# Optimization experiments

Hardware: AMD Instinct MI355X
Metric: run time of the kernel (lower is better)

Reference implementation:

```python
import jax, jax.numpy as jnp
import numpy as np

D_MODEL = 512
N_STATE = 64
EMB_DIM = 512
LN_EPS = 1e-5


def setup_inputs() -> dict:
    key = jax.random.key(0)
    ks = jax.random.split(key, 12)
    B, L, d, N, e = 8, 2048, D_MODEL, N_STATE, EMB_DIM
    x = jax.random.normal(ks[0], (B, L, d), dtype=jnp.float32)
    emb = jax.random.normal(ks[1], (B, e), dtype=jnp.float32)
    # S4D kernel params
    A_real = -0.5 * jnp.ones((d, N), dtype=jnp.float32)
    A_imag = jnp.pi * jnp.broadcast_to(jnp.arange(N, dtype=jnp.float32)[None, :], (d, N))
    C = jax.random.normal(ks[2], (d, N, 2), dtype=jnp.float32) * 0.5
    dt_min, dt_max = 0.001, 0.1
    log_dt = jax.random.uniform(ks[3], (d,), dtype=jnp.float32) * (np.log(dt_max) - np.log(dt_min)) + np.log(dt_min)
    B_ssm = jnp.ones((d, N), dtype=jnp.float32)  # buffer, treated as constant
    # block params
    D_skip = jax.random.normal(ks[4], (d,), dtype=jnp.float32) * 0.01
    ln_gamma = jnp.ones((d,), dtype=jnp.float32)
    ln_beta = jnp.zeros((d,), dtype=jnp.float32)
    lim_out = 1.0 / np.sqrt(d)
    W_out = jax.random.uniform(ks[5], (2 * d, d), dtype=jnp.float32, minval=-lim_out, maxval=lim_out)
    b_out = jax.random.uniform(ks[6], (2 * d,), dtype=jnp.float32, minval=-lim_out, maxval=lim_out)
    lim_f = 1.0 / np.sqrt(e)
    W_film = jax.random.uniform(ks[7], (2 * d, e), dtype=jnp.float32, minval=-lim_f, maxval=lim_f)
    b_film = jax.random.uniform(ks[8], (2 * d,), dtype=jnp.float32, minval=-lim_f, maxval=lim_f)
    return dict(x=x, emb=emb, A_real=A_real, A_imag=A_imag, C=C, log_dt=log_dt,
                B_ssm=B_ssm, D_skip=D_skip, ln_gamma=ln_gamma, ln_beta=ln_beta,
                W_out=W_out, b_out=b_out, W_film=W_film, b_film=b_film)


def reference(x, emb, A_real, A_imag, C, log_dt, B_ssm, D_skip, ln_gamma, ln_beta,
              W_out, b_out, W_film, b_film):
    Bsz, L, d = x.shape
    residual = x
    # LayerNorm
    mu = jnp.mean(x, axis=-1, keepdims=True)
    var = jnp.mean((x - mu) ** 2, axis=-1, keepdims=True)
    xn = (x - mu) * jax.lax.rsqrt(var + LN_EPS) * ln_gamma + ln_beta
    # S4D kernel: K[d,l] = Re( sum_n (C*B)[d,n] * exp(dt*A)[d,n]**l ) * dt[d]
    dt = jnp.exp(log_dt)                                 # (d,)
    A = A_real + 1j * A_imag                             # (d,N)
    dtA = A * dt[:, None]                                # (d,N)
    Cc = (C[..., 0] + 1j * C[..., 1]) * B_ssm            # (d,N) complex
    l = jnp.arange(L, dtype=jnp.float32)
    powers = jnp.exp(dtA[:, :, None] * l)                # (d,N,L) complex, A_bar**l
    K = jnp.einsum('dn,dnl->dl', Cc, powers).real * dt[:, None]  # (d,L)
    # FFT convolution (circular over 2L -> linear)
    x_t = jnp.transpose(xn, (0, 2, 1))                   # (B,d,L)
    K_f = jnp.fft.rfft(K, n=2 * L)                       # (d,L+1)
    x_f = jnp.fft.rfft(x_t, n=2 * L)                     # (B,d,L+1)
    y = jnp.fft.irfft(K_f[None] * x_f, n=2 * L)[..., :L] # (B,d,L)
    y = y + x_t * D_skip[None, :, None]
    y = jnp.transpose(y, (0, 2, 1))                      # (B,L,d)
    # FiLM conditioning
    film = jax.nn.silu(emb) @ W_film.T + b_film          # (B,2d)
    scale, shift = jnp.split(film, 2, axis=-1)
    y = y * (1.0 + scale[:, None, :]) + shift[:, None, :]
    # out_proj: Linear(d,2d) + GLU
    proj = y @ W_out.T + b_out                           # (B,L,2d)
    a, g = jnp.split(proj, 2, axis=-1)
    y = a * jax.nn.sigmoid(g)
    return residual + y
```

## Files before the change

kernel.cpp:

```cpp
#include <hip/hip_runtime.h>
#include <math.h>

typedef __attribute__((ext_vector_type(8))) short bf8v;
typedef __attribute__((ext_vector_type(4))) float f4v;

union BF8 { bf8v v; unsigned short e[8]; };

__device__ __forceinline__ float bf2f(unsigned short u) {
  union { unsigned int i; float f; } c; c.i = ((unsigned int)u) << 16; return c.f;
}
__device__ __forceinline__ unsigned short f2bf(float f) {
  union { float f; unsigned int i; } c; c.f = f;
  return (unsigned short)((c.i + 0x7fffu + ((c.i >> 16) & 1u)) >> 16);
}

__global__ __launch_bounds__(64) void ln_kernel(const float* __restrict__ x,
    const float* __restrict__ gamma, const float* __restrict__ beta,
    unsigned short* __restrict__ xn) {
  const int row = blockIdx.x;
  const int lane = threadIdx.x;
  const float4* xr = (const float4*)(x + (size_t)row * 512);
  const float4 v0 = xr[lane * 2], v1 = xr[lane * 2 + 1];
  float s  = v0.x + v0.y + v0.z + v0.w + v1.x + v1.y + v1.z + v1.w;
  float sq = v0.x*v0.x + v0.y*v0.y + v0.z*v0.z + v0.w*v0.w
           + v1.x*v1.x + v1.y*v1.y + v1.z*v1.z + v1.w*v1.w;
  #pragma unroll
  for (int off = 32; off >= 1; off >>= 1) {
    s  += __shfl_xor(s, off);
    sq += __shfl_xor(sq, off);
  }
  const float mu   = s * (1.f / 512.f);
  const float var  = sq * (1.f / 512.f) - mu * mu;
  const float rstd = rsqrtf(var + 1e-5f);
  const float4* gp = (const float4*)gamma + lane * 2;
  const float4* bp = (const float4*)beta  + lane * 2;
  const float4 g0 = gp[0], g1 = gp[1], bb0 = bp[0], bb1 = bp[1];
  const float o0 = (v0.x - mu) * rstd * g0.x + bb0.x;
  const float o1 = (v0.y - mu) * rstd * g0.y + bb0.y;
  const float o2 = (v0.z - mu) * rstd * g0.z + bb0.z;
  const float o3 = (v0.w - mu) * rstd * g0.w + bb0.w;
  const float o4 = (v1.x - mu) * rstd * g1.x + bb1.x;
  const float o5 = (v1.y - mu) * rstd * g1.y + bb1.y;
  const float o6 = (v1.z - mu) * rstd * g1.z + bb1.z;
  const float o7 = (v1.w - mu) * rstd * g1.w + bb1.w;
  uint4 pk;
  pk.x = (unsigned)f2bf(o0) | ((unsigned)f2bf(o1) << 16);
  pk.y = (unsigned)f2bf(o2) | ((unsigned)f2bf(o3) << 16);
  pk.z = (unsigned)f2bf(o4) | ((unsigned)f2bf(o5) << 16);
  pk.w = (unsigned)f2bf(o6) | ((unsigned)f2bf(o7) << 16);
  ((uint4*)(xn + (size_t)row * 512))[lane] = pk;
}

__global__ __launch_bounds__(256) void film_kernel(const float* __restrict__ emb,
    const float* __restrict__ Wf, const float* __restrict__ bfm,
    float* __restrict__ film) {
  const int gw = blockIdx.x * 4 + (threadIdx.x >> 6);
  const int lane = threadIdx.x & 63;
  const int b = gw >> 10, j = gw & 1023;
  const float4* ep = (const float4*)(emb + (size_t)b * 512) + lane * 2;
  const float4* wp = (const float4*)(Wf + (size_t)j * 512) + lane * 2;
  float acc = 0.f;
  #pragma unroll
  for (int i = 0; i < 2; i++) {
    const float4 e = ep[i], w = wp[i];
    acc += (e.x / (1.f + __expf(-e.x))) * w.x;
    acc += (e.y / (1.f + __expf(-e.y))) * w.y;
    acc += (e.z / (1.f + __expf(-e.z))) * w.z;
    acc += (e.w / (1.f + __expf(-e.w))) * w.w;
  }
  #pragma unroll
  for (int off = 32; off >= 1; off >>= 1) acc += __shfl_xor(acc, off);
  if (lane == 0) film[(size_t)b * 1024 + j] = acc + bfm[j];
}

__global__ __launch_bounds__(256) void wcvt_kernel(const float* __restrict__ W,
    unsigned short* __restrict__ Wb) {
  const int i = blockIdx.x * 256 + threadIdx.x;
  const float4 v = ((const float4*)W)[i];
  uint2 pk;
  pk.x = (unsigned)f2bf(v.x) | ((unsigned)f2bf(v.y) << 16);
  pk.y = (unsigned)f2bf(v.z) | ((unsigned)f2bf(v.w) << 16);
  ((uint2*)Wb)[i] = pk;
}

__global__ __launch_bounds__(256) void tr_kernel(const unsigned short* __restrict__ in,
    unsigned short* __restrict__ out, int R, int C) {
  __shared__ __align__(16) unsigned short t[64 * 72];
  const int c0 = blockIdx.x * 64, r0 = blockIdx.y * 64;
  const int tid = threadIdx.x;
  #pragma unroll
  for (int i = 0; i < 2; i++) {
    const int idx = tid + i * 256;
    const int r = idx >> 3, q = idx & 7;
    const uint4 v = *(const uint4*)(in + (size_t)(r0 + r) * C + c0 + q * 8);
    *(uint4*)&t[r * 72 + ((q ^ (r >> 3)) * 8)] = v;
  }
  __syncthreads();
  #pragma unroll
  for (int i = 0; i < 2; i++) {
    const int idx = tid + i * 256;
    const int c = idx >> 3, g = idx & 7;
    union { unsigned short s[8]; uint4 u; } pk;
    #pragma unroll
    for (int j = 0; j < 8; j++)
      pk.s[j] = t[(g * 8 + j) * 72 + (((c >> 3) ^ g) * 8) + (c & 7)];
    *(uint4*)(out + (size_t)(c0 + c) * R + r0 + g * 8) = pk.u;
  }
}

__global__ __launch_bounds__(256) void ktab_kernel(const float* __restrict__ A_real,
    const float* __restrict__ A_imag, const float* __restrict__ Cc,
    const float* __restrict__ log_dt, const float* __restrict__ B_ssm,
    const float* __restrict__ D_skip, float* __restrict__ Kt) {
  const int d = blockIdx.x * 4 + (threadIdx.x >> 6);
  const int n = threadIdx.x & 63;
  const int dn = d * 64 + n;
  const float dt = __expf(log_dt[d]);
  const float er = __expf(dt * A_real[dn]);
  float sw, cw; __sincosf(dt * A_imag[dn], &sw, &cw);
  const float wre = er * cw, wim = er * sw;
  const float bs = B_ssm[dn] * dt;
  float pre = Cc[dn * 2] * bs, pim = Cc[dn * 2 + 1] * bs;
  const float dsk = D_skip[d];
  for (int tau = 0; tau < 64; tau++) {
    float r = pre;
    #pragma unroll
    for (int off = 32; off >= 1; off >>= 1) r += __shfl_xor(r, off);
    if (n == 0) Kt[d * 64 + tau] = (tau == 0) ? (r + dsk) : r;
    const float nre = pre * wre - pim * wim;
    const float nim = pre * wim + pim * wre;
    pre = nre; pim = nim;
  }
}

__global__ __launch_bounds__(256, 1) void ssm_kernel(
    const unsigned short* __restrict__ xT,
    const float* __restrict__ A_real, const float* __restrict__ A_imag,
    const float* __restrict__ Cc, const float* __restrict__ log_dt,
    const float* __restrict__ B_ssm, const float* __restrict__ Kt,
    const float* __restrict__ film, unsigned short* __restrict__ y2) {
  extern __shared__ char smem[];
  unsigned int*   Eb  = (unsigned int*)smem;
  unsigned short* Ibr = (unsigned short*)(smem + 64 * 258 * 4);
  unsigned short* Ibi = Ibr + 256 * 72;

  const int d = blockIdx.x;
  const int tid = threadIdx.x;
  const int wv = tid >> 6, lane = tid & 63;
  const int n15 = lane & 15, quad = lane >> 4;
  const int j0 = wv * 64;
  const float dt = __expf(log_dt[d]);

  bf8v Xf[4][2];
  #pragma unroll
  for (int ct = 0; ct < 4; ct++)
    #pragma unroll
    for (int kq = 0; kq < 2; kq++) {
      const int j = j0 + ct * 16 + n15;
      Xf[ct][kq] = *(const bf8v*)(xT + (size_t)d * 16384 + j * 64 + kq * 32 + quad * 8);
    }

  {
    f4v Er[4][4], Ei[4][4];
    #pragma unroll
    for (int a = 0; a < 4; a++)
      #pragma unroll
      for (int b2 = 0; b2 < 4; b2++) { Er[a][b2] = (f4v){0,0,0,0}; Ei[a][b2] = (f4v){0,0,0,0}; }
    #pragma unroll
    for (int mt = 0; mt < 4; mt++) {
      const int n = mt * 16 + n15;
      const float ar = dt * A_real[d * 64 + n], ai = dt * A_imag[d * 64 + n];
      #pragma unroll
      for (int kq = 0; kq < 2; kq++) {
        BF8 pr, pi;
        #pragma unroll
        for (int j = 0; j < 8; j++) {
          const float k = (float)(63 - (kq * 32 + quad * 8 + j));
          const float ex = __expf(ar * k);
          float sn, cs; __sincosf(ai * k, &sn, &cs);
          pr.e[j] = f2bf(ex * cs);
          pi.e[j] = f2bf(ex * sn);
        }
        #pragma unroll
        for (int ct = 0; ct < 4; ct++) {
          Er[mt][ct] = __builtin_amdgcn_mfma_f32_16x16x32_bf16(pr.v, Xf[ct][kq], Er[mt][ct], 0, 0, 0);
          Ei[mt][ct] = __builtin_amdgcn_mfma_f32_16x16x32_bf16(pi.v, Xf[ct][kq], Ei[mt][ct], 0, 0, 0);
        }
      }
    }
    #pragma unroll
    for (int mt = 0; mt < 4; mt++)
      #pragma unroll
      for (int ct = 0; ct < 4; ct++)
        #pragma unroll
        for (int i = 0; i < 4; i++) {
          const int row = mt * 16 + quad * 4 + i;
          const int col = j0 + ct * 16 + n15;
          Eb[row * 258 + col] =
              (unsigned)f2bf(Er[mt][ct][i]) | ((unsigned)f2bf(Ei[mt][ct][i]) << 16);
        }
  }
  __syncthreads();

  {
    const int n = tid & 63, bp = tid >> 6;
    const int dn = d * 64 + n;
    const float ex = __expf(dt * A_real[dn] * 64.f);
    float sn, cs; __sincosf(dt * A_imag[dn] * 64.f, &sn, &cs);
    const float w64re = ex * cs, w64im = ex * sn;
    #pragma unroll
    for (int half = 0; half < 2; half++) {
      const int b = bp + half * 4;
      float str = 0.f, sti = 0.f;
      for (int c = 0; c < 32; c++) {
        const int j = b * 32 + c;
        Ibr[j * 72 + n] = f2bf(str);
        Ibi[j * 72 + n] = f2bf(sti);
        const unsigned e = Eb[n * 258 + j];
        const float er2 = bf2f((unsigned short)(e & 0xffffu));
        const float ei2 = bf2f((unsigned short)(e >> 16));
        const float nr = er2 + w64re * str - w64im * sti;
        const float ni = ei2 + w64re * sti + w64im * str;
        str = nr; sti = ni;
      }
    }
  }
  __syncthreads();

  f4v Y[4][4];
  #pragma unroll
  for (int a = 0; a < 4; a++)
    #pragma unroll
    for (int b2 = 0; b2 < 4; b2++) Y[a][b2] = (f4v){0,0,0,0};

  #pragma unroll
  for (int mt = 0; mt < 4; mt++) {
    const int t = mt * 16 + n15;
    #pragma unroll
    for (int kq = 0; kq < 2; kq++) {
      BF8 tf;
      #pragma unroll
      for (int j = 0; j < 8; j++) {
        const int s = kq * 32 + quad * 8 + j;
        tf.e[j] = (s <= t) ? f2bf(Kt[d * 64 + (t - s)]) : (unsigned short)0;
      }
      #pragma unroll
      for (int ct = 0; ct < 4; ct++)
        Y[mt][ct] = __builtin_amdgcn_mfma_f32_16x16x32_bf16(tf.v, Xf[ct][kq], Y[mt][ct], 0, 0, 0);
    }
  }

  #pragma unroll
  for (int kq = 0; kq < 2; kq++) {
    float arj[8], aij[8], c0j[8], c1j[8];
    #pragma unroll
    for (int j = 0; j < 8; j++) {
      const int dn = d * 64 + kq * 32 + quad * 8 + j;
      arj[j] = dt * A_real[dn];
      aij[j] = dt * A_imag[dn];
      const float bs = B_ssm[dn] * dt;
      c0j[j] = Cc[dn * 2] * bs;
      c1j[j] = Cc[dn * 2 + 1] * bs;
    }
    bf8v irf[4], iif[4];
    #pragma unroll
    for (int ct = 0; ct < 4; ct++) {
      const int j = j0 + ct * 16 + n15;
      irf[ct] = *(const bf8v*)&Ibr[j * 72 + kq * 32 + quad * 8];
      iif[ct] = *(const bf8v*)&Ibi[j * 72 + kq * 32 + quad * 8];
    }
    #pragma unroll
    for (int mt = 0; mt < 4; mt++) {
      const int t = mt * 16 + n15;
      BF8 mr, mi;
      #pragma unroll
      for (int j = 0; j < 8; j++) {
        const float k = (float)(t + 1);
        const float ex = __expf(arj[j] * k);
        float sn, cs; __sincosf(aij[j] * k, &sn, &cs);
        mr.e[j] = f2bf(ex * (c0j[j] * cs - c1j[j] * sn));
        mi.e[j] = f2bf(-ex * (c0j[j] * sn + c1j[j] * cs));
      }
      #pragma unroll
      for (int ct = 0; ct < 4; ct++) {
        Y[mt][ct] = __builtin_amdgcn_mfma_f32_16x16x32_bf16(mr.v, irf[ct], Y[mt][ct], 0, 0, 0);
        Y[mt][ct] = __builtin_amdgcn_mfma_f32_16x16x32_bf16(mi.v, iif[ct], Y[mt][ct], 0, 0, 0);
      }
    }
  }

  #pragma unroll
  for (int ct = 0; ct < 4; ct++) {
    const int j = j0 + ct * 16 + n15;
    const int b = j >> 5;
    const float scl = 1.f + film[b * 1024 + d];
    const float shf = film[b * 1024 + 512 + d];
    #pragma unroll
    for (int mt = 0; mt < 4; mt++) {
      union { unsigned short s[4]; uint2 u; } pk;
      #pragma unroll
      for (int i = 0; i < 4; i++)
        pk.s[i] = f2bf(fmaf(Y[mt][ct][i], scl, shf));
      *(uint2*)(y2 + (size_t)d * 16384 + j * 64 + mt * 16 + quad * 4) = pk.u;
    }
  }
}

__global__ __launch_bounds__(256) void gemm_kernel(
    const unsigned short* __restrict__ y2n, const unsigned short* __restrict__ Wb,
    const float* __restrict__ bo, const float* __restrict__ x,
    float* __restrict__ out) {
  __shared__ __align__(16) unsigned short Al[64 * 48];
  __shared__ __align__(16) unsigned short Bl[128 * 48];
  const int m0 = blockIdx.x * 64, ct = blockIdx.y;
  const int tid = threadIdx.x;
  const int wv = tid >> 6, lane = tid & 63;
  const int n15 = lane & 15, quad = lane >> 4;
  f4v acc[2][4];
  #pragma unroll
  for (int hh = 0; hh < 2; hh++)
    #pragma unroll
    for (int t4 = 0; t4 < 4; t4++) acc[hh][t4] = (f4v){0.f, 0.f, 0.f, 0.f};

  const int ar  = tid >> 2;
  const int ak  = (tid & 3) * 8;
  const int cc0 = tid >> 2;
  const int ks  = (tid & 3) * 8;

  for (int kk = 0; kk < 16; kk++) {
    *(uint4*)&Al[ar * 48 + ak] =
        *(const uint4*)(y2n + (size_t)(m0 + ar) * 512 + kk * 32 + ak);
    #pragma unroll
    for (int r = 0; r < 2; r++) {
      const int cc = cc0 + r * 64;
      const int cg = (cc < 64) ? (ct * 64 + cc) : (512 + ct * 64 + (cc - 64));
      *(uint4*)&Bl[cc * 48 + ks] = *(const uint4*)(Wb + (size_t)cg * 512 + kk * 32 + ks);
    }
    __syncthreads();
    const bf8v a = *(const bf8v*)&Al[(wv * 16 + n15) * 48 + quad * 8];
    #pragma unroll
    for (int hh = 0; hh < 2; hh++)
      #pragma unroll
      for (int t4 = 0; t4 < 4; t4++) {
        const bf8v bb = *(const bf8v*)&Bl[(hh * 64 + t4 * 16 + n15) * 48 + quad * 8];
        acc[hh][t4] = __builtin_amdgcn_mfma_f32_16x16x32_bf16(a, bb, acc[hh][t4], 0, 0, 0);
      }
    __syncthreads();
  }
  const int mrow = m0 + wv * 16 + quad * 4;
  #pragma unroll
  for (int t4 = 0; t4 < 4; t4++) {
    const int c = ct * 64 + t4 * 16 + n15;
    const float ba = bo[c], bg = bo[512 + c];
    #pragma unroll
    for (int i = 0; i < 4; i++) {
      const size_t off = (size_t)(mrow + i) * 512 + c;
      const float av = acc[0][t4][i] + ba;
      const float gv = acc[1][t4][i] + bg;
      out[off] = x[off] + av * (1.f / (1.f + __expf(-gv)));
    }
  }
}

extern "C" void kernel_launch(void* const* d_in, const int* in_sizes, int n_in,
                              void* d_out, int out_size, void* d_ws, size_t ws_size,
                              hipStream_t stream) {
  const float* x      = (const float*)d_in[0];
  const float* emb    = (const float*)d_in[1];
  const float* A_real = (const float*)d_in[2];
  const float* A_imag = (const float*)d_in[3];
  const float* C      = (const float*)d_in[4];
  const float* log_dt = (const float*)d_in[5];
  const float* B_ssm  = (const float*)d_in[6];
  const float* D_skip = (const float*)d_in[7];
  const float* gamma  = (const float*)d_in[8];
  const float* beta   = (const float*)d_in[9];
  const float* W_out  = (const float*)d_in[10];
  const float* b_out  = (const float*)d_in[11];
  const float* W_film = (const float*)d_in[12];
  const float* b_film = (const float*)d_in[13];
  float* out = (float*)d_out;

  char* ws = (char*)d_ws;
  float*          film = (float*)ws;
  unsigned short* xn   = (unsigned short*)(ws + 32768);
  unsigned short* xT   = (unsigned short*)(ws + 32768 + 16777216);
  float*          Kt   = (float*)(ws + 32768 + 2 * 16777216);
  unsigned short* Wb   = (unsigned short*)(ws + 32768 + 2 * 16777216 + 131072);
  unsigned short* y2   = xn;
  unsigned short* y2n  = xT;

  film_kernel<<<dim3(2048), dim3(256), 0, stream>>>(emb, W_film, b_film, film);
  ln_kernel<<<dim3(16384), dim3(64), 0, stream>>>(x, gamma, beta, xn);
  wcvt_kernel<<<dim3(512), dim3(256), 0, stream>>>(W_out, Wb);
  ktab_kernel<<<dim3(128), dim3(256), 0, stream>>>(A_real, A_imag, C, log_dt, B_ssm, D_skip, Kt);
  tr_kernel<<<dim3(8, 256), dim3(256), 0, stream>>>(xn, xT, 16384, 512);
  ssm_kernel<<<dim3(512), dim3(256), 139776, stream>>>(xT, A_real, A_imag, C, log_dt,
                                                       B_ssm, Kt, film, y2);
  tr_kernel<<<dim3(256, 8), dim3(256), 0, stream>>>(y2, y2n, 512, 16384);
  gemm_kernel<<<dim3(256, 8), dim3(256), 0, stream>>>(y2n, Wb, b_out, x, out);
}
```

Baseline: 215.2 us.

## Precompute SSM bf16 operand tables, split SSM blocks, retile GEMM with direct LDS loads

A new tab_kernel precomputes, once per channel, the bf16 power matrices (P, M), the Toeplitz kernel tile and the w^64 chunk multipliers in workspace. The SSM kernel now loads these instead of evaluating exp/sincos inline. The SSM kernel is also split into two blocks per channel, each covering four batches, which halves shared memory and registers so two blocks can run per CU. The output GEMM moves to 128-row tiles with global_load_lds direct-to-LDS copies and a higher occupancy hint. The cost is an extra launch plus about 20 MB of table writes and reads, and redundant table loads in each half-block.

```diff
diff --git a/kernel.cpp b/kernel.cpp
--- a/kernel.cpp
+++ b/kernel.cpp
@@ -12,6 +12,11 @@
 __device__ __forceinline__ unsigned short f2bf(float f) {
   union { float f; unsigned int i; } c; c.f = f;
   return (unsigned short)((c.i + 0x7fffu + ((c.i >> 16) & 1u)) >> 16);
+}
+__device__ __forceinline__ void gld16(const unsigned short* g, unsigned short* l) {
+  __builtin_amdgcn_global_load_lds(
+      (const __attribute__((address_space(1))) unsigned int*)g,
+      (__attribute__((address_space(3))) unsigned int*)l, 16, 0, 0);
 }
 
 __global__ __launch_bounds__(64) void ln_kernel(const float* __restrict__ x,
@@ -133,70 +138,125 @@
   }
 }
 
-__global__ __launch_bounds__(256, 1) void ssm_kernel(
-    const unsigned short* __restrict__ xT,
+__global__ __launch_bounds__(256) void tab_kernel(
     const float* __restrict__ A_real, const float* __restrict__ A_imag,
     const float* __restrict__ Cc, const float* __restrict__ log_dt,
     const float* __restrict__ B_ssm, const float* __restrict__ Kt,
+    unsigned short* __restrict__ Pre, unsigned short* __restrict__ Pim,
+    unsigned short* __restrict__ Mre, unsigned short* __restrict__ Mim,
+    unsigned short* __restrict__ Tt, float* __restrict__ W64r, float* __restrict__ W64i) {
+  const int d = blockIdx.x;
+  const int tid = threadIdx.x;
+  const float dt = __expf(log_dt[d]);
+  for (int g = tid; g < 512; g += 256) {
+    const int n = g >> 3, s0 = (g & 7) * 8;
+    const int dn = d * 64 + n;
+    const float ar = dt * A_real[dn], ai = dt * A_imag[dn];
+    union { unsigned short s[8]; uint4 u; } pr, pi;
+    #pragma unroll
+    for (int j = 0; j < 8; j++) {
+      const float k = (float)(63 - (s0 + j));
+      const float ex = __expf(ar * k);
+      float sn, cs; __sincosf(ai * k, &sn, &cs);
+      pr.s[j] = f2bf(ex * cs); pi.s[j] = f2bf(ex * sn);
+    }
+    *(uint4*)(Pre + (size_t)d * 4096 + n * 64 + s0) = pr.u;
+    *(uint4*)(Pim + (size_t)d * 4096 + n * 64 + s0) = pi.u;
+  }
+  for (int g = tid; g < 512; g += 256) {
+    const int t = g >> 3, n0 = (g & 7) * 8;
+    union { unsigned short s[8]; uint4 u; } mr, mi;
+    #pragma unroll
+    for (int j = 0; j < 8; j++) {
+      const int dn = d * 64 + n0 + j;
+      const float ar = dt * A_real[dn], ai = dt * A_imag[dn];
+      const float bs = B_ssm[dn] * dt;
+      const float c0 = Cc[dn * 2] * bs, c1 = Cc[dn * 2 + 1] * bs;
+      const float k = (float)(t + 1);
+      const float ex = __expf(ar * k);
+      float sn, cs; __sincosf(ai * k, &sn, &cs);
+      mr.s[j] = f2bf(ex * (c0 * cs - c1 * sn));
+      mi.s[j] = f2bf(-ex * (c0 * sn + c1 * cs));
+    }
+    *(uint4*)(Mre + (size_t)d * 4096 + t * 64 + n0) = mr.u;
+    *(uint4*)(Mim + (size_t)d * 4096 + t * 64 + n0) = mi.u;
+  }
+  for (int g = tid; g < 512; g += 256) {
+    const int t = g >> 3, s0 = (g & 7) * 8;
+    union { unsigned short s[8]; uint4 u; } tv;
+    #pragma unroll
+    for (int j = 0; j < 8; j++) {
+      const int s = s0 + j;
+      tv.s[j] = (s <= t) ? f2bf(Kt[d * 64 + (t - s)]) : (unsigned short)0;
+    }
+    *(uint4*)(Tt + (size_t)d * 4096 + t * 64 + s0) = tv.u;
+  }
+  if (tid < 64) {
+    const int dn = d * 64 + tid;
+    const float ex = __expf(dt * A_real[dn] * 64.f);
+    float sn, cs; __sincosf(dt * A_imag[dn] * 64.f, &sn, &cs);
+    W64r[d * 64 + tid] = ex * cs;
+    W64i[d * 64 + tid] = ex * sn;
+  }
+}
+
+__global__ __launch_bounds__(256, 2) void ssm_kernel(
+    const unsigned short* __restrict__ xT,
+    const unsigned short* __restrict__ Pre, const unsigned short* __restrict__ Pim,
+    const unsigned short* __restrict__ Mre, const unsigned short* __restrict__ Mim,
+    const unsigned short* __restrict__ Tt,
+    const float* __restrict__ W64r, const float* __restrict__ W64i,
     const float* __restrict__ film, unsigned short* __restrict__ y2) {
   extern __shared__ char smem[];
   unsigned int*   Eb  = (unsigned int*)smem;
-  unsigned short* Ibr = (unsigned short*)(smem + 64 * 258 * 4);
-  unsigned short* Ibi = Ibr + 256 * 72;
-
-  const int d = blockIdx.x;
+  unsigned short* Ibr = (unsigned short*)(smem + 64 * 133 * 4);
+  unsigned short* Ibi = Ibr + 128 * 72;
+
+  const int bx = blockIdx.x;
+  const int d = bx & 511, h = bx >> 9;
   const int tid = threadIdx.x;
   const int wv = tid >> 6, lane = tid & 63;
   const int n15 = lane & 15, quad = lane >> 4;
-  const int j0 = wv * 64;
-  const float dt = __expf(log_dt[d]);
-
-  bf8v Xf[4][2];
-  #pragma unroll
-  for (int ct = 0; ct < 4; ct++)
+  const int j0 = wv * 32;
+  const int jg0 = h * 128;
+  const size_t dtab = (size_t)d * 4096;
+
+  bf8v Xf[2][2];
+  #pragma unroll
+  for (int ct = 0; ct < 2; ct++)
     #pragma unroll
     for (int kq = 0; kq < 2; kq++) {
       const int j = j0 + ct * 16 + n15;
-      Xf[ct][kq] = *(const bf8v*)(xT + (size_t)d * 16384 + j * 64 + kq * 32 + quad * 8);
+      Xf[ct][kq] = *(const bf8v*)(xT + (size_t)d * 16384 + (jg0 + j) * 64 + kq * 32 + quad * 8);
     }
 
   {
-    f4v Er[4][4], Ei[4][4];
+    f4v Er[4][2], Ei[4][2];
     #pragma unroll
     for (int a = 0; a < 4; a++)
       #pragma unroll
-      for (int b2 = 0; b2 < 4; b2++) { Er[a][b2] = (f4v){0,0,0,0}; Ei[a][b2] = (f4v){0,0,0,0}; }
-    #pragma unroll
-    for (int mt = 0; mt < 4; mt++) {
-      const int n = mt * 16 + n15;
-      const float ar = dt * A_real[d * 64 + n], ai = dt * A_imag[d * 64 + n];
+      for (int b2 = 0; b2 < 2; b2++) { Er[a][b2] = (f4v){0,0,0,0}; Ei[a][b2] = (f4v){0,0,0,0}; }
+    #pragma unroll
+    for (int mt = 0; mt < 4; mt++)
       #pragma unroll
       for (int kq = 0; kq < 2; kq++) {
-        BF8 pr, pi;
+        const bf8v pr = *(const bf8v*)(Pre + dtab + (mt * 16 + n15) * 64 + kq * 32 + quad * 8);
+        const bf8v pi = *(const bf8v*)(Pim + dtab + (mt * 16 + n15) * 64 + kq * 32 + quad * 8);
         #pragma unroll
-        for (int j = 0; j < 8; j++) {
-          const float k = (float)(63 - (kq * 32 + quad * 8 + j));
-          const float ex = __expf(ar * k);
-          float sn, cs; __sincosf(ai * k, &sn, &cs);
-          pr.e[j] = f2bf(ex * cs);
-          pi.e[j] = f2bf(ex * sn);
-        }
-        #pragma unroll
-        for (int ct = 0; ct < 4; ct++) {
-          Er[mt][ct] = __builtin_amdgcn_mfma_f32_16x16x32_bf16(pr.v, Xf[ct][kq], Er[mt][ct], 0, 0, 0);
-          Ei[mt][ct] = __builtin_amdgcn_mfma_f32_16x16x32_bf16(pi.v, Xf[ct][kq], Ei[mt][ct], 0, 0, 0);
+        for (int ct = 0; ct < 2; ct++) {
+          Er[mt][ct] = __builtin_amdgcn_mfma_f32_16x16x32_bf16(pr, Xf[ct][kq], Er[mt][ct], 0, 0, 0);
+          Ei[mt][ct] = __builtin_amdgcn_mfma_f32_16x16x32_bf16(pi, Xf[ct][kq], Ei[mt][ct], 0, 0, 0);
         }
       }
-    }
     #pragma unroll
     for (int mt = 0; mt < 4; mt++)
       #pragma unroll
-      for (int ct = 0; ct < 4; ct++)
+      for (int ct = 0; ct < 2; ct++)
         #pragma unroll
         for (int i = 0; i < 4; i++) {
           const int row = mt * 16 + quad * 4 + i;
           const int col = j0 + ct * 16 + n15;
-          Eb[row * 258 + col] =
+          Eb[row * 133 + col] =
               (unsigned)f2bf(Er[mt][ct][i]) | ((unsigned)f2bf(Ei[mt][ct][i]) << 16);
         }
   }
@@ -204,95 +264,67 @@
 
   {
     const int n = tid & 63, bp = tid >> 6;
-    const int dn = d * 64 + n;
-    const float ex = __expf(dt * A_real[dn] * 64.f);
-    float sn, cs; __sincosf(dt * A_imag[dn] * 64.f, &sn, &cs);
-    const float w64re = ex * cs, w64im = ex * sn;
-    #pragma unroll
-    for (int half = 0; half < 2; half++) {
-      const int b = bp + half * 4;
-      float str = 0.f, sti = 0.f;
-      for (int c = 0; c < 32; c++) {
-        const int j = b * 32 + c;
-        Ibr[j * 72 + n] = f2bf(str);
-        Ibi[j * 72 + n] = f2bf(sti);
-        const unsigned e = Eb[n * 258 + j];
-        const float er2 = bf2f((unsigned short)(e & 0xffffu));
-        const float ei2 = bf2f((unsigned short)(e >> 16));
-        const float nr = er2 + w64re * str - w64im * sti;
-        const float ni = ei2 + w64re * sti + w64im * str;
-        str = nr; sti = ni;
-      }
+    const float wre = W64r[d * 64 + n], wim = W64i[d * 64 + n];
+    unsigned int eb[32];
+    #pragma unroll
+    for (int c = 0; c < 32; c++) eb[c] = Eb[n * 133 + bp * 32 + c];
+    float str = 0.f, sti = 0.f;
+    #pragma unroll
+    for (int c = 0; c < 32; c++) {
+      const int j = bp * 32 + c;
+      Ibr[j * 72 + n] = f2bf(str);
+      Ibi[j * 72 + n] = f2bf(sti);
+      const float er = bf2f((unsigned short)(eb[c] & 0xffffu));
+      const float ei = bf2f((unsigned short)(eb[c] >> 16));
+      const float nr = er + wre * str - wim * sti;
+      const float ni = ei + wre * sti + wim * str;
+      str = nr; sti = ni;
     }
   }
   __syncthreads();
 
-  f4v Y[4][4];
+  f4v Y[4][2];
   #pragma unroll
   for (int a = 0; a < 4; a++)
     #pragma unroll
-    for (int b2 = 0; b2 < 4; b2++) Y[a][b2] = (f4v){0,0,0,0};
-
-  #pragma unroll
-  for (int mt = 0; mt < 4; mt++) {
-    const int t = mt * 16 + n15;
+    for (int b2 = 0; b2 < 2; b2++) Y[a][b2] = (f4v){0,0,0,0};
+
+  #pragma unroll
+  for (int mt = 0; mt < 4; mt++)
     #pragma unroll
     for (int kq = 0; kq < 2; kq++) {
-      BF8 tf;
-      #pragma unroll
-      for (int j = 0; j < 8; j++) {
-        const int s = kq * 32 + quad * 8 + j;
-        tf.e[j] = (s <= t) ? f2bf(Kt[d * 64 + (t - s)]) : (unsigned short)0;
-      }
-      #pragma unroll
-      for (int ct = 0; ct < 4; ct++)
-        Y[mt][ct] = __builtin_amdgcn_mfma_f32_16x16x32_bf16(tf.v, Xf[ct][kq], Y[mt][ct], 0, 0, 0);
-    }
-  }
+      const bf8v tf = *(const bf8v*)(Tt + dtab + (mt * 16 + n15) * 64 + kq * 32 + quad * 8);
+      #pragma unroll
+      for (int ct = 0; ct < 2; ct++)
+        Y[mt][ct] = __builtin_amdgcn_mfma_f32_16x16x32_bf16(tf, Xf[ct][kq], Y[mt][ct], 0, 0, 0);
+    }
 
   #pragma unroll
   for (int kq = 0; kq < 2; kq++) {
-    float arj[8], aij[8], c0j[8], c1j[8];
-    #pragma unroll
-    for (int j = 0; j < 8; j++) {
-      const int dn = d * 64 + kq * 32 + quad * 8 + j;
-      arj[j] = dt * A_real[dn];
-      aij[j] = dt * A_imag[dn];
-      const float bs = B_ssm[dn] * dt;
-      c0j[j] = Cc[dn * 2] * bs;
-      c1j[j] = Cc[dn * 2 + 1] * bs;
-    }
-    bf8v irf[4], iif[4];
-    #pragma unroll
-    for (int ct = 0; ct < 4; ct++) {
+    bf8v irf[2], iif[2];
+    #pragma unroll
+    for (int ct = 0; ct < 2; ct++) {
       const int j = j0 + ct * 16 + n15;
       irf[ct] = *(const bf8v*)&Ibr[j * 72 + kq * 32 + quad * 8];
       iif[ct] = *(const bf8v*)&Ibi[j * 72 + kq * 32 + quad * 8];
     }
     #pragma unroll
     for (int mt = 0; mt < 4; mt++) {
-      const int t = mt * 16 + n15;
-      BF8 mr, mi;
-      #pragma unroll
-      for (int j = 0; j < 8; j++) {
-        const float k = (float)(t + 1);
-        const float ex = __expf(arj[j] * k);
-        float sn, cs; __sincosf(aij[j] * k, &sn, &cs);
-        mr.e[j] = f2bf(ex * (c0j[j] * cs - c1j[j] * sn));
-        mi.e[j] = f2bf(-ex * (c0j[j] * sn + c1j[j] * cs));
+      const bf8v mr = *(const bf8v*)(Mre + dtab + (mt * 16 + n15) * 64 + kq * 32 + quad * 8);
+      const bf8v mi = *(const bf8v*)(Mim + dtab + (mt * 16 + n15) * 64 + kq * 32 + quad * 8);
+      #pragma unroll
+      for (int ct = 0; ct < 2; ct++) {
+        Y[mt][ct] = __builtin_amdgcn_mfma_f32_16x16x32_bf16(mr, irf[ct], Y[mt][ct], 0, 0, 0);
+        Y[mt][ct] = __builtin_amdgcn_mfma_f32_16x16x32_bf16(mi, iif[ct], Y[mt][ct], 0, 0, 0);
       }
-      #pragma unroll
-      for (int ct = 0; ct < 4; ct++) {
-        Y[mt][ct] = __builtin_amdgcn_mfma_f32_16x16x32_bf16(mr.v, irf[ct], Y[mt][ct], 0, 0, 0);
-        Y[mt][ct] = __builtin_amdgcn_mfma_f32_16x16x32_bf16(mi.v, iif[ct], Y[mt][ct], 0, 0, 0);
-      }
-    }
-  }
-
-  #pragma unroll
-  for (int ct = 0; ct < 4; ct++) {
-    const int j = j0 + ct * 16 + n15;
-    const int b = j >> 5;
+    }
+  }
+
+  #pragma unroll
+  for (int ct = 0; ct < 2; ct++) {
+    const int jl = j0 + ct * 16 + n15;
+    const int jglob = jg0 + jl;
+    const int b = jglob >> 5;
     const float scl = 1.f + film[b * 1024 + d];
     const float shf = film[b * 1024 + 512 + d];
     #pragma unroll
@@ -301,63 +333,63 @@
       #pragma unroll
       for (int i = 0; i < 4; i++)
         pk.s[i] = f2bf(fmaf(Y[mt][ct][i], scl, shf));
-      *(uint2*)(y2 + (size_t)d * 16384 + j * 64 + mt * 16 + quad * 4) = pk.u;
-    }
-  }
-}
-
-__global__ __launch_bounds__(256) void gemm_kernel(
+      *(uint2*)(y2 + (size_t)d * 16384 + jglob * 64 + mt * 16 + quad * 4) = pk.u;
+    }
+  }
+}
+
+__global__ __launch_bounds__(256, 3) void gemm_kernel(
     const unsigned short* __restrict__ y2n, const unsigned short* __restrict__ Wb,
     const float* __restrict__ bo, const float* __restrict__ x,
     float* __restrict__ out) {
-  __shared__ __align__(16) unsigned short Al[64 * 48];
-  __shared__ __align__(16) unsigned short Bl[128 * 48];
-  const int m0 = blockIdx.x * 64, ct = blockIdx.y;
+  __shared__ __align__(16) unsigned short Al[128 * 32];
+  __shared__ __align__(16) unsigned short Bl[128 * 32];
+  const int m0 = blockIdx.x * 128, ct = blockIdx.y;
   const int tid = threadIdx.x;
   const int wv = tid >> 6, lane = tid & 63;
   const int n15 = lane & 15, quad = lane >> 4;
-  f4v acc[2][4];
-  #pragma unroll
-  for (int hh = 0; hh < 2; hh++)
-    #pragma unroll
-    for (int t4 = 0; t4 < 4; t4++) acc[hh][t4] = (f4v){0.f, 0.f, 0.f, 0.f};
-
-  const int ar  = tid >> 2;
-  const int ak  = (tid & 3) * 8;
-  const int cc0 = tid >> 2;
-  const int ks  = (tid & 3) * 8;
+  const int srow = lane >> 2;
+  const int sk = (lane & 3) * 8;
+
+  f4v acc[2][8];
+  #pragma unroll
+  for (int mi = 0; mi < 2; mi++)
+    #pragma unroll
+    for (int t4 = 0; t4 < 8; t4++) acc[mi][t4] = (f4v){0.f, 0.f, 0.f, 0.f};
 
   for (int kk = 0; kk < 16; kk++) {
-    *(uint4*)&Al[ar * 48 + ak] =
-        *(const uint4*)(y2n + (size_t)(m0 + ar) * 512 + kk * 32 + ak);
-    #pragma unroll
-    for (int r = 0; r < 2; r++) {
-      const int cc = cc0 + r * 64;
-      const int cg = (cc < 64) ? (ct * 64 + cc) : (512 + ct * 64 + (cc - 64));
-      *(uint4*)&Bl[cc * 48 + ks] = *(const uint4*)(Wb + (size_t)cg * 512 + kk * 32 + ks);
+    #pragma unroll
+    for (int i = 0; i < 2; i++) {
+      const int row = wv * 32 + i * 16 + srow;
+      gld16(y2n + (size_t)(m0 + row) * 512 + kk * 32 + sk, Al + wv * 1024 + i * 512);
+      const int c = (row < 64) ? (ct * 64 + row) : (512 + ct * 64 + (row - 64));
+      gld16(Wb + (size_t)c * 512 + kk * 32 + sk, Bl + wv * 1024 + i * 512);
     }
     __syncthreads();
-    const bf8v a = *(const bf8v*)&Al[(wv * 16 + n15) * 48 + quad * 8];
-    #pragma unroll
-    for (int hh = 0; hh < 2; hh++)
-      #pragma unroll
-      for (int t4 = 0; t4 < 4; t4++) {
-        const bf8v bb = *(const bf8v*)&Bl[(hh * 64 + t4 * 16 + n15) * 48 + quad * 8];
-        acc[hh][t4] = __builtin_amdgcn_mfma_f32_16x16x32_bf16(a, bb, acc[hh][t4], 0, 0, 0);
+    bf8v a0 = *(const bf8v*)&Al[(wv * 32 + n15) * 32 + quad * 8];
+    bf8v a1 = *(const bf8v*)&Al[(wv * 32 + 16 + n15) * 32 + quad * 8];
+    #pragma unroll
+    for (int t4 = 0; t4 < 8; t4++) {
+      const bf8v bb = *(const bf8v*)&Bl[(t4 * 16 + n15) * 32 + quad * 8];
+      acc[0][t4] = __builtin_amdgcn_mfma_f32_16x16x32_bf16(a0, bb, acc[0][t4], 0, 0, 0);
+      acc[1][t4] = __builtin_amdgcn_mfma_f32_16x16x32_bf16(a1, bb, acc[1][t4], 0, 0, 0);
+    }
+    __syncthreads();
+  }
+  #pragma unroll
+  for (int mi = 0; mi < 2; mi++) {
+    const int mrow = m0 + wv * 32 + mi * 16 + quad * 4;
+    #pragma unroll
+    for (int t4 = 0; t4 < 4; t4++) {
+      const int c = ct * 64 + t4 * 16 + n15;
+      const float ba = bo[c], bg = bo[512 + c];
+      #pragma unroll
+      for (int i = 0; i < 4; i++) {
+        const size_t off = (size_t)(mrow + i) * 512 + c;
+        const float av = acc[mi][t4][i] + ba;
+        const float gv = acc[mi][t4 + 4][i] + bg;
+        out[off] = x[off] + av * (1.f / (1.f + __expf(-gv)));
       }
-    __syncthreads();
-  }
-  const int mrow = m0 + wv * 16 + quad * 4;
-  #pragma unroll
-  for (int t4 = 0; t4 < 4; t4++) {
-    const int c = ct * 64 + t4 * 16 + n15;
-    const float ba = bo[c], bg = bo[512 + c];
-    #pragma unroll
-    for (int i = 0; i < 4; i++) {
-      const size_t off = (size_t)(mrow + i) * 512 + c;
-      const float av = acc[0][t4][i] + ba;
-      const float gv = acc[1][t4][i] + bg;
-      out[off] = x[off] + av * (1.f / (1.f + __expf(-gv)));
     }
   }
 }
@@ -382,11 +414,19 @@
   float* out = (float*)d_out;
 
   char* ws = (char*)d_ws;
-  float*          film = (float*)ws;
-  unsigned short* xn   = (unsigned short*)(ws + 32768);
-  unsigned short* xT   = (unsigned short*)(ws + 32768 + 16777216);
-  float*          Kt   = (float*)(ws + 32768 + 2 * 16777216);
-  unsigned short* Wb   = (unsigned short*)(ws + 32768 + 2 * 16777216 + 131072);
+  size_t o = 0;
+  float*          film = (float*)(ws + o);          o += 32768;
+  unsigned short* xn   = (unsigned short*)(ws + o); o += 16777216;
+  unsigned short* xT   = (unsigned short*)(ws + o); o += 16777216;
+  float*          Kt   = (float*)(ws + o);          o += 131072;
+  unsigned short* Wb   = (unsigned short*)(ws + o); o += 1048576;
+  unsigned short* Pre  = (unsigned short*)(ws + o); o += 4194304;
+  unsigned short* Pim  = (unsigned short*)(ws + o); o += 4194304;
+  unsigned short* Mre  = (unsigned short*)(ws + o); o += 4194304;
+  unsigned short* Mim  = (unsigned short*)(ws + o); o += 4194304;
+  unsigned short* Tt   = (unsigned short*)(ws + o); o += 4194304;
+  float*          W64r = (float*)(ws + o);          o += 131072;
+  float*          W64i = (float*)(ws + o);          o += 131072;
   unsigned short* y2   = xn;
   unsigned short* y2n  = xT;
 
@@ -394,9 +434,11 @@
   ln_kernel<<<dim3(16384), dim3(64), 0, stream>>>(x, gamma, beta, xn);
   wcvt_kernel<<<dim3(512), dim3(256), 0, stream>>>(W_out, Wb);
   ktab_kernel<<<dim3(128), dim3(256), 0, stream>>>(A_real, A_imag, C, log_dt, B_ssm, D_skip, Kt);
+  tab_kernel<<<dim3(512), dim3(256), 0, stream>>>(A_real, A_imag, C, log_dt, B_ssm, Kt,
+                                                  Pre, Pim, Mre, Mim, Tt, W64r, W64i);
   tr_kernel<<<dim3(8, 256), dim3(256), 0, stream>>>(xn, xT, 16384, 512);
-  ssm_kernel<<<dim3(512), dim3(256), 139776, stream>>>(xT, A_real, A_imag, C, log_dt,
-                                                       B_ssm, Kt, film, y2);
+  ssm_kernel<<<dim3(1024), dim3(256), 70912, stream>>>(xT, Pre, Pim, Mre, Mim, Tt,
+                                                       W64r, W64i, film, y2);
   tr_kernel<<<dim3(256, 8), dim3(256), 0, stream>>>(y2, y2n, 512, 16384);
-  gemm_kernel<<<dim3(256, 8), dim3(256), 0, stream>>>(y2n, Wb, b_out, x, out);
-}
+  gemm_kernel<<<dim3(128, 8), dim3(256), 0, stream>>>(y2n, Wb, b_out, x, out);
+}
```

Result: faster. 205.3 us (-4.6%).
